# Kernel tuning notes

Measured on AMD Instinct MI355X. Metric: run time of the kernel, lower is better.

Reference implementation:

```python
import jax, jax.numpy as jnp
import numpy as np

N = 100000   # nodes
E = 1600000  # edges (before self-loops)
D = 128      # in_feats
H = 128      # n_hidden


def setup_inputs() -> dict:
    key = jax.random.key(0)
    k = jax.random.split(key, 6)
    x = jax.random.normal(k[0], (N, D), dtype=jnp.float32)
    src = jax.random.randint(k[1], (E,), 0, N, dtype=jnp.int32)
    dst = jax.random.randint(k[2], (E,), 0, N, dtype=jnp.int32)
    W1 = jax.random.normal(k[3], (D, H), dtype=jnp.float32) / np.float32(np.sqrt(D))
    b1 = jnp.zeros((H,), jnp.float32)
    W2 = jax.random.normal(k[4], (H, H), dtype=jnp.float32) / np.float32(np.sqrt(H))
    b2 = jnp.zeros((H,), jnp.float32)
    return {"x": x, "src": src, "dst": dst, "W1": W1, "b1": b1, "W2": W2, "b2": b2}


def _gcn(x, src, dst, W1, b1, W2, b2):
    n = x.shape[0]
    # add_self_loop(g)
    loops = jnp.arange(n, dtype=src.dtype)
    s = jnp.concatenate([src, loops])
    d = jnp.concatenate([dst, loops])
    ones = jnp.ones((s.shape[0],), dtype=x.dtype)
    deg_out = jax.ops.segment_sum(ones, s, num_segments=n)  # src out-degree
    deg_in = jax.ops.segment_sum(ones, d, num_segments=n)   # dst in-degree
    # DGL GraphConv norm='both': D_out^{-1/2} on source side, D_in^{-1/2} on dest side
    norm_out = jax.lax.rsqrt(jnp.maximum(deg_out, 1.0))[:, None]
    norm_in = jax.lax.rsqrt(jnp.maximum(deg_in, 1.0))[:, None]

    def layer(h, W, b):
        h = h * norm_out                                   # [n, f]
        agg = jax.ops.segment_sum(h[s], d, num_segments=n)  # gather + scatter-add over edges
        return (agg * norm_in) @ W + b

    h = layer(x, W1, b1)
    # dropout p=0 -> identity
    h = layer(h, W2, b2)
    return h


def reference(x, src, dst, W1, b1, W2, b2):
    return _gcn(x, src, dst, W1, b1, W2, b2)
```

## Files before the change

kernel.cpp:

```cpp
#include <hip/hip_runtime.h>

#define FD 128
#define SHIFT 10
#define BNODES 1024
#define NBK 128
#define CHUNK 4096
#define ST 512

typedef unsigned int u32;
typedef unsigned short u16;
typedef unsigned char u8;
typedef __attribute__((ext_vector_type(8))) short short8;
typedef __attribute__((ext_vector_type(4))) float f32x4;
typedef __attribute__((ext_vector_type(4))) u32 u32x4;

__device__ inline u16 f2bf(float f) {
  u32 u = __float_as_uint(f);
  u += 0x7fffu + ((u >> 16) & 1u);
  return (u16)(u >> 16);
}
__device__ inline float bf2f(u16 h) { return __uint_as_float((u32)h << 16); }

__global__ __launch_bounds__(512) void k_hist(const int* __restrict__ src,
                                              const int* __restrict__ dst,
                                              int* __restrict__ bcntD,
                                              int* __restrict__ bcntS,
                                              int e, int n, int nbuck) {
  __shared__ int shD[NBK];
  __shared__ int shS[NBK];
  int tid = threadIdx.x;
  if (tid < NBK) { shD[tid] = 0; shS[tid] = 0; }
  __syncthreads();
  int total = e + n;
  for (int t = blockIdx.x * blockDim.x + tid; t < total; t += gridDim.x * blockDim.x) {
    if (t < e) {
      atomicAdd(&shD[dst[t] >> SHIFT], 1);
      atomicAdd(&shS[src[t] >> SHIFT], 1);
    } else {
      atomicAdd(&shD[(t - e) >> SHIFT], 1);
    }
  }
  __syncthreads();
  if (tid < nbuck) {
    if (shD[tid]) atomicAdd(&bcntD[tid], shD[tid]);
    if (shS[tid]) atomicAdd(&bcntS[tid], shS[tid]);
  }
}

__global__ __launch_bounds__(NBK) void k_bscan(
    const int* __restrict__ bcntD, const int* __restrict__ bcntS,
    int* __restrict__ bbaseD, int* __restrict__ bcurD,
    int* __restrict__ bbaseS, int* __restrict__ bcurS,
    int nbuck, int totalD, int totalS) {
  __shared__ int shD[NBK];
  __shared__ int shS[NBK];
  int tid = threadIdx.x;
  int vD = (tid < nbuck) ? bcntD[tid] : 0;
  int vS = (tid < nbuck) ? bcntS[tid] : 0;
  shD[tid] = vD; shS[tid] = vS;
  __syncthreads();
  for (int off = 1; off < NBK; off <<= 1) {
    int aD = (tid >= off) ? shD[tid - off] : 0;
    int aS = (tid >= off) ? shS[tid - off] : 0;
    __syncthreads();
    shD[tid] += aD; shS[tid] += aS;
    __syncthreads();
  }
  if (tid < nbuck) {
    int exD = shD[tid] - vD; bbaseD[tid] = exD; bcurD[tid] = exD;
    int exS = shS[tid] - vS; bbaseS[tid] = exS; bcurS[tid] = exS;
  }
  if (tid == 0) { bbaseD[nbuck] = totalD; bbaseS[nbuck] = totalS; }
}

__global__ __launch_bounds__(ST) void k_scatter(
    const int* __restrict__ src, const int* __restrict__ dst,
    int* __restrict__ bcurD, int* __restrict__ bcurS,
    u32* __restrict__ pairs, u16* __restrict__ pairs2,
    int e, int n, int nbuck) {
  __shared__ int histD[NBK], exclD[NBK], gbaseD[NBK], rankD[NBK];
  __shared__ int histS[NBK], exclS[NBK], gbaseS[NBK], rankS[NBK];
  __shared__ u32 stgv[CHUNK];
  __shared__ u8  stgb[CHUNK];
  __shared__ u16 stg2[CHUNK];
  __shared__ u8  stg2b[CHUNK];
  int tid = threadIdx.x;
  int c0 = blockIdx.x * CHUNK;
  int total = e + n;
  if (tid < NBK) { histD[tid] = 0; histS[tid] = 0; }
  __syncthreads();
  u32 pv_[8]; int bD_[8], bS_[8]; bool v_[8], vs_[8];
  #pragma unroll
  for (int i = 0; i < 8; ++i) {
    int t = c0 + i * ST + tid;
    v_[i] = (t < total);
    vs_[i] = (t < e);
    pv_[i] = 0; bD_[i] = 0; bS_[i] = 0;
    if (v_[i]) {
      int s, d;
      if (vs_[i]) { s = src[t]; d = dst[t]; }
      else        { s = t - e;  d = s; }
      pv_[i] = ((u32)(d & (BNODES - 1)) << 22) | (u32)s;
      bD_[i] = d >> SHIFT;
      atomicAdd(&histD[bD_[i]], 1);
      if (vs_[i]) { bS_[i] = s >> SHIFT; atomicAdd(&histS[bS_[i]], 1); }
    }
  }
  __syncthreads();
  int hD = 0, hS = 0;
  if (tid < NBK) { hD = histD[tid]; hS = histS[tid]; }
  __syncthreads();
  for (int off = 1; off < NBK; off <<= 1) {
    int aD = 0, aS = 0;
    if (tid < NBK && tid >= off) { aD = histD[tid - off]; aS = histS[tid - off]; }
    __syncthreads();
    if (tid < NBK) { histD[tid] += aD; histS[tid] += aS; }
    __syncthreads();
  }
  if (tid < NBK) {
    int exD = histD[tid] - hD; exclD[tid] = exD; rankD[tid] = exD;
    int exS = histS[tid] - hS; exclS[tid] = exS; rankS[tid] = exS;
    gbaseD[tid] = (tid < nbuck && hD > 0) ? atomicAdd(&bcurD[tid], hD) : 0;
    gbaseS[tid] = (tid < nbuck && hS > 0) ? atomicAdd(&bcurS[tid], hS) : 0;
  }
  __syncthreads();
  #pragma unroll
  for (int i = 0; i < 8; ++i) {
    if (v_[i]) {
      int p = atomicAdd(&rankD[bD_[i]], 1);
      stgv[p] = pv_[i];
      stgb[p] = (u8)bD_[i];
    }
    if (vs_[i]) {
      int p = atomicAdd(&rankS[bS_[i]], 1);
      stg2[p] = (u16)(pv_[i] & (BNODES - 1));
      stg2b[p] = (u8)bS_[i];
    }
  }
  __syncthreads();
  int V = min(CHUNK, total - c0);
  for (int j = tid; j < V; j += ST) {
    int b = stgb[j];
    pairs[gbaseD[b] + (j - exclD[b])] = stgv[j];
  }
  int V2 = min(CHUNK, e - c0);
  for (int j = tid; j < V2; j += ST) {
    int b = stg2b[j];
    pairs2[gbaseS[b] + (j - exclS[b])] = stg2[j];
  }
}

__global__ __launch_bounds__(1024) void k_build(
    const u32* __restrict__ pairs, const int* __restrict__ bbase,
    const u16* __restrict__ pairs2, const int* __restrict__ bbaseS,
    int* __restrict__ rp, int* __restrict__ col,
    float* __restrict__ nin, float* __restrict__ nout,
    int n, int nbuck, int total) {
  __shared__ int cnt[BNODES];
  __shared__ int off_[BNODES];
  __shared__ int cur[BNODES];
  int tid = threadIdx.x;
  if (blockIdx.x >= (unsigned)nbuck) {
    int b = blockIdx.x - nbuck;
    int base = bbaseS[b], end = bbaseS[b + 1];
    cnt[tid] = 0;
    __syncthreads();
    for (int t = base + tid; t < end; t += 1024)
      atomicAdd(&cnt[(int)pairs2[t]], 1);
    __syncthreads();
    int node = (b << SHIFT) + tid;
    if (node < n) nout[node] = rsqrtf((float)(cnt[tid] + 1));
    return;
  }
  int b = blockIdx.x;
  int base = bbase[b], end = bbase[b + 1];
  int node0 = b << SHIFT;
  cnt[tid] = 0;
  __syncthreads();
  for (int t = base + tid; t < end; t += 1024)
    atomicAdd(&cnt[(int)(pairs[t] >> 22)], 1);
  __syncthreads();
  int c = cnt[tid];
  off_[tid] = c;
  __syncthreads();
  for (int off = 1; off < BNODES; off <<= 1) {
    int add = (tid >= off) ? off_[tid - off] : 0;
    __syncthreads();
    off_[tid] += add;
    __syncthreads();
  }
  int ex = off_[tid] - c;
  int node = node0 + tid;
  if (node < n) {
    rp[node] = base + ex;
    nin[node] = rsqrtf((float)c);
  }
  if (b == nbuck - 1 && tid == 0) rp[n] = total;
  cur[tid] = ex;
  __syncthreads();
  for (int t = base + tid; t < end; t += 1024) {
    u32 pr = pairs[t];
    int p = atomicAdd(&cur[(int)(pr >> 22)], 1);
    col[base + p] = (int)(pr & 0x3FFFFFu);
  }
}

__global__ __launch_bounds__(256) void k_prescale(
    const float* __restrict__ x, const float* __restrict__ nout,
    u32* __restrict__ xs, int n) {
  int tot = (n + 1) * 64;
  const float2* xv = (const float2*)x;
  for (int idx = blockIdx.x * blockDim.x + threadIdx.x; idx < tot;
       idx += gridDim.x * blockDim.x) {
    int row = idx >> 6;
    if (row >= n) { xs[idx] = 0; }
    else {
      float w = nout[row];
      float2 v = xv[idx];
      xs[idx] = (u32)f2bf(v.x * w) | ((u32)f2bf(v.y * w) << 16);
    }
  }
}

__global__ void k_prepw(const float* __restrict__ W1, u32* __restrict__ wf1hi,
                        u32* __restrict__ wf1lo,
                        const float* __restrict__ W2, u32* __restrict__ wf2hi,
                        u32* __restrict__ wf2lo) {
  int gi = blockIdx.x * 256 + threadIdx.x;
  int i = gi & 8191;
  const float* W = (gi < 8192) ? W1 : W2;
  u32* wfhi = (gi < 8192) ? wf1hi : wf2hi;
  u32* wflo = (gi < 8192) ? wf1lo : wf2lo;
  int m = i & 3, l = (i >> 2) & 63, f = i >> 8;
  int kt = f & 3, nt = f >> 2;
  int k0 = kt * 32 + ((l >> 4) << 3) + 2 * m;
  int c = nt * 16 + (l & 15);
  float w0 = W[k0 * FD + c], w1 = W[(k0 + 1) * FD + c];
  u16 h0 = f2bf(w0), h1 = f2bf(w1);
  u16 l0 = f2bf(w0 - bf2f(h0)), l1 = f2bf(w1 - bf2f(h1));
  wfhi[i] = (u32)h0 | ((u32)h1 << 16);
  wflo[i] = (u32)l0 | ((u32)l1 << 16);
}

__global__ __launch_bounds__(256, 8) void k_layer(
    const u32* __restrict__ hs, const int* __restrict__ rp,
    const int* __restrict__ col, const float* __restrict__ nin,
    const u32* __restrict__ wfhi, const u32* __restrict__ wflo,
    const float* __restrict__ bias, const float* __restrict__ nout,
    float* __restrict__ fout, u16* __restrict__ hsout, int n, int mode) {
  __shared__ u32 As[1024];
  int tid = threadIdx.x;
  int lane = tid & 63;
  int wv = tid >> 6;
  int g = lane >> 4, ch = lane & 15;
  int r0 = blockIdx.x * 16;
  int lr = wv * 4 + g;
  int r = r0 + lr;
  bool valid = (r < n);

  int e0 = 0, e1 = 0;
  if (valid) { e0 = rp[r]; e1 = rp[r + 1]; }
  int m = e1 - e0;
  m = max(m, __shfl_xor(m, 16, 64));
  m = max(m, __shfl_xor(m, 32, 64));
  int trips = (m + 7) >> 3;
  float acc[8] = {0.f, 0.f, 0.f, 0.f, 0.f, 0.f, 0.f, 0.f};
  const u32x4* hv = (const u32x4*)hs;
  int em1 = (e1 > 0) ? (e1 - 1) : 0;
  for (int it = 0; it < trips; ++it) {
    int tb = e0 + it * 8;
    u32x4 buf[8];
    #pragma unroll
    for (int u = 0; u < 8; ++u) {
      int idx = tb + u;
      int s = col[min(idx, em1)];
      s = (idx < e1) ? s : n;
      buf[u] = hv[(size_t)s * 16 + ch];
    }
    #pragma unroll
    for (int u = 0; u < 8; ++u)
      #pragma unroll
      for (int j = 0; j < 4; ++j) {
        u32 x = buf[u][j];
        acc[2 * j]     += __uint_as_float(x << 16);
        acc[2 * j + 1] += __uint_as_float(x & 0xFFFF0000u);
      }
  }
  float wi = valid ? nin[r] : 0.f;
  u32 hi[4];
  #pragma unroll
  for (int j = 0; j < 4; ++j) {
    float v0 = acc[2 * j] * wi, v1 = acc[2 * j + 1] * wi;
    hi[j] = (u32)f2bf(v0) | ((u32)f2bf(v1) << 16);
  }
  int sch = ch ^ (lr & 7);
  u32x4 hq = {hi[0], hi[1], hi[2], hi[3]};
  *(u32x4*)(As + lr * 64 + sch * 4) = hq;
  __syncthreads();

  short8 afh[4];
  int arow = lane & 15;
  #pragma unroll
  for (int kt = 0; kt < 4; ++kt) {
    int boff = arow * 256 + ((kt * 64 + (lane >> 4) * 16) ^ ((arow & 7) << 4));
    afh[kt] = *(const short8*)((const char*)As + boff);
  }
  #pragma unroll
  for (int q = 0; q < 2; ++q) {
    int nt = wv * 2 + q;
    f32x4 oacc = {0.f, 0.f, 0.f, 0.f};
    #pragma unroll
    for (int kt = 0; kt < 4; ++kt) {
      int f = nt * 4 + kt;
      short8 wh = *(const short8*)(wfhi + (size_t)(f * 64 + lane) * 4);
      short8 wl = *(const short8*)(wflo + (size_t)(f * 64 + lane) * 4);
      oacc = __builtin_amdgcn_mfma_f32_16x16x32_bf16(afh[kt], wh, oacc, 0, 0, 0);
      oacc = __builtin_amdgcn_mfma_f32_16x16x32_bf16(afh[kt], wl, oacc, 0, 0, 0);
    }
    int c = nt * 16 + (lane & 15);
    float bv = bias[c];
    int rbase = r0 + (lane >> 4) * 4;
    if (mode == 0) {
      #pragma unroll
      for (int j = 0; j < 4; ++j) {
        int row = rbase + j;
        if (row < n) fout[(size_t)row * FD + c] = oacc[j] + bv;
      }
    } else {
      #pragma unroll
      for (int j = 0; j < 4; ++j) {
        int row = rbase + j;
        if (row < n) hsout[(size_t)row * FD + c] = f2bf((oacc[j] + bv) * nout[row]);
      }
    }
  }
}

extern "C" void kernel_launch(void* const* d_in, const int* in_sizes, int n_in,
                              void* d_out, int out_size, void* d_ws, size_t ws_size,
                              hipStream_t stream) {
  const float* x  = (const float*)d_in[0];
  const int* src  = (const int*)d_in[1];
  const int* dst  = (const int*)d_in[2];
  const float* W1 = (const float*)d_in[3];
  const float* b1 = (const float*)d_in[4];
  const float* W2 = (const float*)d_in[5];
  const float* b2 = (const float*)d_in[6];
  float* out = (float*)d_out;

  int n = in_sizes[0] / FD;
  int e = in_sizes[1];
  int total = e + n;
  int nbuck = (n + BNODES - 1) >> SHIFT;

  char* ws = (char*)d_ws;
  size_t off = 0;
  auto alloc = [&](size_t bytes) -> void* {
    void* p = ws + off;
    off += (bytes + 255) / 256 * 256;
    return p;
  };
  u32* xs    = (u32*)alloc((size_t)(n + 16) * 64 * 4);
  u32* pairs = xs;
  u16* h1s   = (u16*)alloc((size_t)(n + 16) * FD * 2);
  u16* pairs2 = (u16*)alloc((size_t)e * 2 + 256);
  int* col   = (int*)alloc((size_t)total * 4 + 256);
  int* rp    = (int*)alloc((size_t)(n + 1) * 4);
  float* nin  = (float*)alloc((size_t)n * 4);
  float* nout = (float*)alloc((size_t)n * 4);
  int* bcntD  = (int*)alloc(NBK * 4);
  int* bcntS  = (int*)alloc(NBK * 4);
  int* bbaseD = (int*)alloc((NBK + 1) * 4);
  int* bbaseS = (int*)alloc((NBK + 1) * 4);
  int* bcurD  = (int*)alloc(NBK * 4);
  int* bcurS  = (int*)alloc(NBK * 4);
  u32* wf1hi  = (u32*)alloc(8192 * 4);
  u32* wf1lo  = (u32*)alloc(8192 * 4);
  u32* wf2hi  = (u32*)alloc(8192 * 4);
  u32* wf2lo  = (u32*)alloc(8192 * 4);

  hipMemsetAsync(bcntD, 0, (size_t)NBK * 4 * 2, stream);
  hipMemsetAsync(h1s + (size_t)n * FD, 0, FD * 2, stream);

  k_hist<<<256, 512, 0, stream>>>(src, dst, bcntD, bcntS, e, n, nbuck);
  k_bscan<<<1, NBK, 0, stream>>>(bcntD, bcntS, bbaseD, bcurD, bbaseS, bcurS,
                                 nbuck, total, e);
  k_scatter<<<(total + CHUNK - 1) / CHUNK, ST, 0, stream>>>(
      src, dst, bcurD, bcurS, pairs, pairs2, e, n, nbuck);
  k_build<<<2 * nbuck, 1024, 0, stream>>>(pairs, bbaseD, pairs2, bbaseS,
                                          rp, col, nin, nout, n, nbuck, total);
  k_prepw<<<64, 256, 0, stream>>>(W1, wf1hi, wf1lo, W2, wf2hi, wf2lo);
  k_prescale<<<2048, 256, 0, stream>>>(x, nout, xs, n);

  int lgrid = (n + 15) / 16;
  k_layer<<<lgrid, 256, 0, stream>>>(xs, rp, col, nin, wf1hi, wf1lo, b1, nout,
                                     nullptr, h1s, n, 1);
  k_layer<<<lgrid, 256, 0, stream>>>((const u32*)h1s, rp, col, nin, wf2hi, wf2lo,
                                     b2, nout, out, nullptr, n, 0);
}
```

Before: 235.9 us.

## Prefetch next edge indices, widen gather unroll, stage layer-1 output via LDS

The gather loop now handles 12 edges per trip instead of 8 and software-prefetches the next trip's column indices while the current feature rows are in flight. A scheduling barrier keeps those loads ahead of the accumulation. The bf16 layer-1 output is written into shared memory and then stored as coalesced 16-byte row chunks instead of scattered 2-byte stores. Dropping the occupancy hint from launch_bounds and holding more registers may lower occupancy. Wider trips also waste more padded loads on low-degree rows.

Measured after the change: 228.5 us. 3.1% less time.

```diff
diff --git a/kernel.cpp b/kernel.cpp
--- a/kernel.cpp
+++ b/kernel.cpp
@@ -6,6 +6,7 @@
 #define NBK 128
 #define CHUNK 4096
 #define ST 512
+#define NE 12
 
 typedef unsigned int u32;
 typedef unsigned short u16;
@@ -242,12 +243,12 @@
   wflo[i] = (u32)l0 | ((u32)l1 << 16);
 }
 
-__global__ __launch_bounds__(256, 8) void k_layer(
+__global__ __launch_bounds__(256) void k_layer(
     const u32* __restrict__ hs, const int* __restrict__ rp,
     const int* __restrict__ col, const float* __restrict__ nin,
     const u32* __restrict__ wfhi, const u32* __restrict__ wflo,
     const float* __restrict__ bias, const float* __restrict__ nout,
-    float* __restrict__ fout, u16* __restrict__ hsout, int n, int mode) {
+    float* __restrict__ fout, u32* __restrict__ hsout, int n, int mode) {
   __shared__ u32 As[1024];
   int tid = threadIdx.x;
   int lane = tid & 63;
@@ -263,28 +264,35 @@
   int m = e1 - e0;
   m = max(m, __shfl_xor(m, 16, 64));
   m = max(m, __shfl_xor(m, 32, 64));
-  int trips = (m + 7) >> 3;
+  int trips = (m + NE - 1) / NE;
   float acc[8] = {0.f, 0.f, 0.f, 0.f, 0.f, 0.f, 0.f, 0.f};
   const u32x4* hv = (const u32x4*)hs;
   int em1 = (e1 > 0) ? (e1 - 1) : 0;
+
+  int cs[NE], csn[NE];
+  #pragma unroll
+  for (int u = 0; u < NE; ++u) cs[u] = col[min(e0 + u, em1)];
   for (int it = 0; it < trips; ++it) {
-    int tb = e0 + it * 8;
-    u32x4 buf[8];
+    int tb = e0 + it * NE;
+    u32x4 buf[NE];
     #pragma unroll
-    for (int u = 0; u < 8; ++u) {
-      int idx = tb + u;
-      int s = col[min(idx, em1)];
-      s = (idx < e1) ? s : n;
+    for (int u = 0; u < NE; ++u) {
+      int s = (tb + u < e1) ? cs[u] : n;
       buf[u] = hv[(size_t)s * 16 + ch];
     }
     #pragma unroll
-    for (int u = 0; u < 8; ++u)
+    for (int u = 0; u < NE; ++u) csn[u] = col[min(tb + NE + u, em1)];
+    __builtin_amdgcn_sched_barrier(0);
+    #pragma unroll
+    for (int u = 0; u < NE; ++u)
       #pragma unroll
       for (int j = 0; j < 4; ++j) {
         u32 x = buf[u][j];
         acc[2 * j]     += __uint_as_float(x << 16);
         acc[2 * j + 1] += __uint_as_float(x & 0xFFFF0000u);
       }
+    #pragma unroll
+    for (int u = 0; u < NE; ++u) cs[u] = csn[u];
   }
   float wi = valid ? nin[r] : 0.f;
   u32 hi[4];
@@ -305,6 +313,8 @@
     int boff = arow * 256 + ((kt * 64 + (lane >> 4) * 16) ^ ((arow & 7) << 4));
     afh[kt] = *(const short8*)((const char*)As + boff);
   }
+  __syncthreads();
+
   #pragma unroll
   for (int q = 0; q < 2; ++q) {
     int nt = wv * 2 + q;
@@ -330,9 +340,17 @@
       #pragma unroll
       for (int j = 0; j < 4; ++j) {
         int row = rbase + j;
-        if (row < n) hsout[(size_t)row * FD + c] = f2bf((oacc[j] + bv) * nout[row]);
+        float w = (row < n) ? nout[row] : 0.f;
+        ((u16*)As)[(row - r0) * 128 + c] = f2bf((oacc[j] + bv) * w);
       }
     }
+  }
+  if (mode == 1) {
+    __syncthreads();
+    int row = tid >> 4, chk = tid & 15;
+    if (r0 + row < n)
+      *(u32x4*)(hsout + (size_t)(r0 + row) * 64 + chk * 4) =
+          *(const u32x4*)(As + row * 64 + chk * 4);
   }
 }
 
@@ -362,7 +380,7 @@
   };
   u32* xs    = (u32*)alloc((size_t)(n + 16) * 64 * 4);
   u32* pairs = xs;
-  u16* h1s   = (u16*)alloc((size_t)(n + 16) * FD * 2);
+  u32* h1s   = (u32*)alloc((size_t)(n + 16) * 64 * 4);
   u16* pairs2 = (u16*)alloc((size_t)e * 2 + 256);
   int* col   = (int*)alloc((size_t)total * 4 + 256);
   int* rp    = (int*)alloc((size_t)(n + 1) * 4);
@@ -380,7 +398,7 @@
   u32* wf2lo  = (u32*)alloc(8192 * 4);
 
   hipMemsetAsync(bcntD, 0, (size_t)NBK * 4 * 2, stream);
-  hipMemsetAsync(h1s + (size_t)n * FD, 0, FD * 2, stream);
+  hipMemsetAsync(h1s + (size_t)n * 64, 0, FD * 2, stream);
 
   k_hist<<<256, 512, 0, stream>>>(src, dst, bcntD, bcntS, e, n, nbuck);
   k_bscan<<<1, NBK, 0, stream>>>(bcntD, bcntS, bbaseD, bcurD, bbaseS, bcurS,
@@ -395,6 +413,6 @@
   int lgrid = (n + 15) / 16;
   k_layer<<<lgrid, 256, 0, stream>>>(xs, rp, col, nin, wf1hi, wf1lo, b1, nout,
                                      nullptr, h1s, n, 1);
-  k_layer<<<lgrid, 256, 0, stream>>>((const u32*)h1s, rp, col, nin, wf2hi, wf2lo,
+  k_layer<<<lgrid, 256, 0, stream>>>(h1s, rp, col, nin, wf2hi, wf2lo,
                                      b2, nout, out, nullptr, n, 0);
 }
```

## Reorder GCN layers to transform-then-aggregate with separate GEMM and aggregation kernels

Applied to the files above, without the earlier changes.

Changes each layer from aggregate-then-multiply to multiply-then-aggregate. The first GEMM now runs on raw x, launched before graph construction, and the output-degree scaling moves into separate scale and GEMM epilogues. Bias is added in a new standalone aggregation kernel, and the second-layer GEMM scales by out-degree before the final aggregation. This unfuses the previous combined gather+MFMA kernel into several passes, which adds extra full-feature reads and writes in exchange for simpler aggregation kernels with better occupancy.

After: 244.5 us. 1.04x slower.

```diff
diff --git a/kernel.cpp b/kernel.cpp
--- a/kernel.cpp
+++ b/kernel.cpp
@@ -202,23 +202,6 @@
     u32 pr = pairs[t];
     int p = atomicAdd(&cur[(int)(pr >> 22)], 1);
     col[base + p] = (int)(pr & 0x3FFFFFu);
-  }
-}
-
-__global__ __launch_bounds__(256) void k_prescale(
-    const float* __restrict__ x, const float* __restrict__ nout,
-    u32* __restrict__ xs, int n) {
-  int tot = (n + 1) * 64;
-  const float2* xv = (const float2*)x;
-  for (int idx = blockIdx.x * blockDim.x + threadIdx.x; idx < tot;
-       idx += gridDim.x * blockDim.x) {
-    int row = idx >> 6;
-    if (row >= n) { xs[idx] = 0; }
-    else {
-      float w = nout[row];
-      float2 v = xv[idx];
-      xs[idx] = (u32)f2bf(v.x * w) | ((u32)f2bf(v.y * w) << 16);
-    }
   }
 }
 
@@ -242,22 +225,91 @@
   wflo[i] = (u32)l0 | ((u32)l1 << 16);
 }
 
-__global__ __launch_bounds__(256, 8) void k_layer(
+__global__ __launch_bounds__(256) void k_gemmx(
+    const float* __restrict__ x,
+    const u32* __restrict__ wfhi, const u32* __restrict__ wflo,
+    u32* __restrict__ tout, int n) {
+  __shared__ u32 As[4096];
+  int tid = threadIdx.x;
+  int lane = tid & 63;
+  int mt = tid >> 6;
+  int r0 = blockIdx.x * 64;
+
+  #pragma unroll
+  for (int it = 0; it < 16; ++it) {
+    int w = it * 256 + tid;
+    int row = w >> 6, u = w & 63;
+    int grow = r0 + row;
+    float2 v = make_float2(0.f, 0.f);
+    if (grow < n) v = *(const float2*)(x + (size_t)grow * FD + u * 2);
+    As[row * 64 + (u ^ ((row & 7) << 2))] = (u32)f2bf(v.x) | ((u32)f2bf(v.y) << 16);
+  }
+  __syncthreads();
+
+  short8 afh[4];
+  int arow = mt * 16 + (lane & 15);
+  #pragma unroll
+  for (int kt = 0; kt < 4; ++kt) {
+    int boff = arow * 256 + ((kt * 64 + (lane >> 4) * 16) ^ ((arow & 7) << 4));
+    afh[kt] = *(const short8*)((const char*)As + boff);
+  }
+  __syncthreads();
+
+  for (int nt = 0; nt < 8; ++nt) {
+    f32x4 oacc = {0.f, 0.f, 0.f, 0.f};
+    #pragma unroll
+    for (int kt = 0; kt < 4; ++kt) {
+      int f = nt * 4 + kt;
+      short8 wh = *(const short8*)(wfhi + (size_t)(f * 64 + lane) * 4);
+      short8 wl = *(const short8*)(wflo + (size_t)(f * 64 + lane) * 4);
+      oacc = __builtin_amdgcn_mfma_f32_16x16x32_bf16(afh[kt], wh, oacc, 0, 0, 0);
+      oacc = __builtin_amdgcn_mfma_f32_16x16x32_bf16(afh[kt], wl, oacc, 0, 0, 0);
+    }
+    int c = nt * 16 + (lane & 15);
+    #pragma unroll
+    for (int j = 0; j < 4; ++j) {
+      int lrow = mt * 16 + (lane >> 4) * 4 + j;
+      ((u16*)As)[lrow * 128 + c] = f2bf(oacc[j]);
+    }
+  }
+  __syncthreads();
+  #pragma unroll
+  for (int it = 0; it < 4; ++it) {
+    int ci = it * 256 + tid;
+    int lrow = ci >> 4, chk = ci & 15;
+    int row = r0 + lrow;
+    if (row < n)
+      *(u32x4*)(tout + (size_t)row * 64 + chk * 4) =
+          *(const u32x4*)(As + lrow * 64 + chk * 4);
+  }
+}
+
+__global__ __launch_bounds__(256) void k_scale(
+    const u32* __restrict__ t1, const float* __restrict__ nout,
+    u32* __restrict__ y1, int n) {
+  int tot = (n + 1) * 64;
+  for (int idx = blockIdx.x * blockDim.x + threadIdx.x; idx < tot;
+       idx += gridDim.x * blockDim.x) {
+    int row = idx >> 6;
+    if (row >= n) { y1[idx] = 0; continue; }
+    float w = nout[row];
+    u32 v = t1[idx];
+    float lo = __uint_as_float(v << 16) * w;
+    float hi = __uint_as_float(v & 0xFFFF0000u) * w;
+    y1[idx] = (u32)f2bf(lo) | ((u32)f2bf(hi) << 16);
+  }
+}
+
+__global__ __launch_bounds__(256) void k_agg(
     const u32* __restrict__ hs, const int* __restrict__ rp,
     const int* __restrict__ col, const float* __restrict__ nin,
-    const u32* __restrict__ wfhi, const u32* __restrict__ wflo,
-    const float* __restrict__ bias, const float* __restrict__ nout,
-    float* __restrict__ fout, u16* __restrict__ hsout, int n, int mode) {
-  __shared__ u32 As[1024];
-  int tid = threadIdx.x;
-  int lane = tid & 63;
-  int wv = tid >> 6;
+    const float* __restrict__ bias,
+    float* __restrict__ fout, u32* __restrict__ hsout, int n, int mode) {
+  int wid = (blockIdx.x * 256 + threadIdx.x) >> 6;
+  int lane = threadIdx.x & 63;
   int g = lane >> 4, ch = lane & 15;
-  int r0 = blockIdx.x * 16;
-  int lr = wv * 4 + g;
-  int r = r0 + lr;
+  int r = wid * 4 + g;
   bool valid = (r < n);
-
   int e0 = 0, e1 = 0;
   if (valid) { e0 = rp[r]; e1 = rp[r + 1]; }
   int m = e1 - e0;
@@ -286,28 +338,62 @@
         acc[2 * j + 1] += __uint_as_float(x & 0xFFFF0000u);
       }
   }
-  float wi = valid ? nin[r] : 0.f;
-  u32 hi[4];
-  #pragma unroll
-  for (int j = 0; j < 4; ++j) {
-    float v0 = acc[2 * j] * wi, v1 = acc[2 * j + 1] * wi;
-    hi[j] = (u32)f2bf(v0) | ((u32)f2bf(v1) << 16);
-  }
-  int sch = ch ^ (lr & 7);
-  u32x4 hq = {hi[0], hi[1], hi[2], hi[3]};
-  *(u32x4*)(As + lr * 64 + sch * 4) = hq;
+  if (!valid) return;
+  float wi = nin[r];
+  float4 b0 = *(const float4*)(bias + ch * 8);
+  float4 b1v = *(const float4*)(bias + ch * 8 + 4);
+  float v[8];
+  v[0] = acc[0] * wi + b0.x;  v[1] = acc[1] * wi + b0.y;
+  v[2] = acc[2] * wi + b0.z;  v[3] = acc[3] * wi + b0.w;
+  v[4] = acc[4] * wi + b1v.x; v[5] = acc[5] * wi + b1v.y;
+  v[6] = acc[6] * wi + b1v.z; v[7] = acc[7] * wi + b1v.w;
+  if (mode == 0) {
+    *(float4*)(fout + (size_t)r * FD + ch * 8)     = make_float4(v[0], v[1], v[2], v[3]);
+    *(float4*)(fout + (size_t)r * FD + ch * 8 + 4) = make_float4(v[4], v[5], v[6], v[7]);
+  } else {
+    u32 hi[4];
+    #pragma unroll
+    for (int j = 0; j < 4; ++j)
+      hi[j] = (u32)f2bf(v[2 * j]) | ((u32)f2bf(v[2 * j + 1]) << 16);
+    int sch = ch ^ (r & 7);
+    u32x4 hq = {hi[0], hi[1], hi[2], hi[3]};
+    *(u32x4*)(hsout + (size_t)r * 64 + sch * 4) = hq;
+  }
+}
+
+__global__ __launch_bounds__(256) void k_gemm2(
+    const u32* __restrict__ ahi,
+    const u32* __restrict__ wfhi, const u32* __restrict__ wflo,
+    const float* __restrict__ nout, u32* __restrict__ yout, int n) {
+  __shared__ u32 As[4096];
+  int tid = threadIdx.x;
+  int lane = tid & 63;
+  int mt = tid >> 6;
+  int r0 = blockIdx.x * 64;
+
+  const u32x4* gh = (const u32x4*)(ahi + (size_t)r0 * 64);
+  u32x4* sh_ = (u32x4*)As;
+  #pragma unroll
+  for (int t = 0; t < 4; ++t) sh_[t * 256 + tid] = gh[t * 256 + tid];
   __syncthreads();
 
   short8 afh[4];
-  int arow = lane & 15;
+  int arow = mt * 16 + (lane & 15);
   #pragma unroll
   for (int kt = 0; kt < 4; ++kt) {
     int boff = arow * 256 + ((kt * 64 + (lane >> 4) * 16) ^ ((arow & 7) << 4));
     afh[kt] = *(const short8*)((const char*)As + boff);
   }
-  #pragma unroll
-  for (int q = 0; q < 2; ++q) {
-    int nt = wv * 2 + q;
+  __syncthreads();
+
+  float wout[4];
+  #pragma unroll
+  for (int j = 0; j < 4; ++j) {
+    int row = r0 + mt * 16 + (lane >> 4) * 4 + j;
+    wout[j] = (row < n) ? nout[row] : 0.f;
+  }
+
+  for (int nt = 0; nt < 8; ++nt) {
     f32x4 oacc = {0.f, 0.f, 0.f, 0.f};
     #pragma unroll
     for (int kt = 0; kt < 4; ++kt) {
@@ -318,21 +404,21 @@
       oacc = __builtin_amdgcn_mfma_f32_16x16x32_bf16(afh[kt], wl, oacc, 0, 0, 0);
     }
     int c = nt * 16 + (lane & 15);
-    float bv = bias[c];
-    int rbase = r0 + (lane >> 4) * 4;
-    if (mode == 0) {
-      #pragma unroll
-      for (int j = 0; j < 4; ++j) {
-        int row = rbase + j;
-        if (row < n) fout[(size_t)row * FD + c] = oacc[j] + bv;
-      }
-    } else {
-      #pragma unroll
-      for (int j = 0; j < 4; ++j) {
-        int row = rbase + j;
-        if (row < n) hsout[(size_t)row * FD + c] = f2bf((oacc[j] + bv) * nout[row]);
-      }
-    }
+    #pragma unroll
+    for (int j = 0; j < 4; ++j) {
+      int lrow = mt * 16 + (lane >> 4) * 4 + j;
+      ((u16*)As)[lrow * 128 + c] = f2bf(oacc[j] * wout[j]);
+    }
+  }
+  __syncthreads();
+  #pragma unroll
+  for (int it = 0; it < 4; ++it) {
+    int ci = it * 256 + tid;
+    int lrow = ci >> 4, chk = ci & 15;
+    int row = r0 + lrow;
+    if (row < n)
+      *(u32x4*)(yout + (size_t)row * 64 + chk * 4) =
+          *(const u32x4*)(As + lrow * 64 + chk * 4);
   }
 }
 
@@ -360,10 +446,15 @@
     off += (bytes + 255) / 256 * 256;
     return p;
   };
-  u32* xs    = (u32*)alloc((size_t)(n + 16) * 64 * 4);
-  u32* pairs = xs;
-  u16* h1s   = (u16*)alloc((size_t)(n + 16) * FD * 2);
-  u16* pairs2 = (u16*)alloc((size_t)e * 2 + 256);
+  u32* bufA  = (u32*)alloc((size_t)(n + 16) * 64 * 4);
+  u32* t1bf  = bufA;
+  u32* y2    = bufA;
+  u32* bufB  = (u32*)alloc((size_t)(n + 16) * 64 * 4);
+  u32* pairs = bufB;
+  u32* y1    = bufB;
+  u32* bufC  = (u32*)alloc((size_t)(n + 64) * 64 * 4);
+  u16* pairs2 = (u16*)bufC;
+  u32* h1bf  = bufC;
   int* col   = (int*)alloc((size_t)total * 4 + 256);
   int* rp    = (int*)alloc((size_t)(n + 1) * 4);
   float* nin  = (float*)alloc((size_t)n * 4);
@@ -380,7 +471,11 @@
   u32* wf2lo  = (u32*)alloc(8192 * 4);
 
   hipMemsetAsync(bcntD, 0, (size_t)NBK * 4 * 2, stream);
-  hipMemsetAsync(h1s + (size_t)n * FD, 0, FD * 2, stream);
+  hipMemsetAsync(bufA + (size_t)n * 64, 0, 64 * 4, stream);
+
+  int ggrid = (n + 63) / 64;
+  k_prepw<<<64, 256, 0, stream>>>(W1, wf1hi, wf1lo, W2, wf2hi, wf2lo);
+  k_gemmx<<<ggrid, 256, 0, stream>>>(x, wf1hi, wf1lo, t1bf, n);
 
   k_hist<<<256, 512, 0, stream>>>(src, dst, bcntD, bcntS, e, n, nbuck);
   k_bscan<<<1, NBK, 0, stream>>>(bcntD, bcntS, bbaseD, bcurD, bbaseS, bcurS,
@@ -389,12 +484,11 @@
       src, dst, bcurD, bcurS, pairs, pairs2, e, n, nbuck);
   k_build<<<2 * nbuck, 1024, 0, stream>>>(pairs, bbaseD, pairs2, bbaseS,
                                           rp, col, nin, nout, n, nbuck, total);
-  k_prepw<<<64, 256, 0, stream>>>(W1, wf1hi, wf1lo, W2, wf2hi, wf2lo);
-  k_prescale<<<2048, 256, 0, stream>>>(x, nout, xs, n);
-
-  int lgrid = (n + 15) / 16;
-  k_layer<<<lgrid, 256, 0, stream>>>(xs, rp, col, nin, wf1hi, wf1lo, b1, nout,
-                                     nullptr, h1s, n, 1);
-  k_layer<<<lgrid, 256, 0, stream>>>((const u32*)h1s, rp, col, nin, wf2hi, wf2lo,
-                                     b2, nout, out, nullptr, n, 0);
-}
+
+  k_scale<<<2048, 256, 0, stream>>>(t1bf, nout, y1, n);
+
+  int agrid = (n + 15) / 16;
+  k_agg<<<agrid, 256, 0, stream>>>(y1, rp, col, nin, b1, nullptr, h1bf, n, 1);
+  k_gemm2<<<ggrid, 256, 0, stream>>>(h1bf, wf2hi, wf2lo, nout, y2, n);
+  k_agg<<<agrid, 256, 0, stream>>>(y2, rp, col, nin, b2, out, nullptr, n, 0);
+}
```
